# Kernel optimization log

Measured on AMD Instinct MI355X. Metric: run time of the kernel, lower is better.

The kernel has to match this reference:

```python
import jax, jax.numpy as jnp
import numpy as np

N = 50000
E = 500000
R = 8
IN_DIM = 128
HID = 128
NUM_CLASSES = 16
NUM_GRAPHS = 64


def setup_inputs() -> dict:
    key = jax.random.key(0)
    ks = jax.random.split(key, 12)
    x = jax.random.normal(ks[0], (N, IN_DIM), dtype=jnp.float32)
    edge_index = jax.random.randint(ks[1], (2, E), 0, N)
    edge_type = jax.random.randint(ks[2], (E,), 0, R)
    batch = jnp.sort(jax.random.randint(ks[3], (N,), 0, NUM_GRAPHS))
    s = 1.0 / np.sqrt(IN_DIM)
    W1 = jax.random.uniform(ks[4], (R, IN_DIM, HID), minval=-s, maxval=s, dtype=jnp.float32)
    root1 = jax.random.uniform(ks[5], (IN_DIM, HID), minval=-s, maxval=s, dtype=jnp.float32)
    b1 = jnp.zeros((HID,), jnp.float32)
    s2 = 1.0 / np.sqrt(HID)
    W2 = jax.random.uniform(ks[6], (R, HID, HID), minval=-s2, maxval=s2, dtype=jnp.float32)
    root2 = jax.random.uniform(ks[7], (HID, HID), minval=-s2, maxval=s2, dtype=jnp.float32)
    b2 = jnp.zeros((HID,), jnp.float32)
    linW = jax.random.uniform(ks[8], (HID, NUM_CLASSES), minval=-s2, maxval=s2, dtype=jnp.float32)
    linb = jnp.zeros((NUM_CLASSES,), jnp.float32)
    return {"x": x, "edge_index": edge_index, "edge_type": edge_type, "batch": batch,
            "W1": W1, "root1": root1, "b1": b1, "W2": W2, "root2": root2, "b2": b2,
            "linW": linW, "linb": linb}


def rgcn_conv(x, src, dst, rel, W, root, b):
    # Per-relation transform of ALL nodes once: [R, N, H] (avoids per-edge weight gather)
    xW = jnp.einsum('nd,rdh->rnh', x, W)
    msg = xW[rel, src]                      # [E, H] gather per edge
    # PyG RGCNConv default aggr='mean': mean over neighbors per (dst, relation)
    seg = dst * R + rel                     # composite segment id
    cnt = jax.ops.segment_sum(jnp.ones((msg.shape[0],), msg.dtype), seg, num_segments=N * R)
    norm = 1.0 / jnp.maximum(cnt, 1.0)
    msg = msg * norm[seg][:, None]
    agg = jax.ops.segment_sum(msg, dst, num_segments=N)  # sum over relations folds in
    return agg + x @ root + b


def global_mean_pool(x, batch):
    sums = jax.ops.segment_sum(x, batch, num_segments=NUM_GRAPHS)
    cnt = jax.ops.segment_sum(jnp.ones((x.shape[0],), x.dtype), batch, num_segments=NUM_GRAPHS)
    return sums / jnp.maximum(cnt, 1.0)[:, None]


def reference(x, edge_index, edge_type, batch, W1, root1, b1, W2, root2, b2, linW, linb):
    src, dst = edge_index[0], edge_index[1]
    h = jax.nn.relu(rgcn_conv(x, src, dst, edge_type, W1, root1, b1))
    h = jax.nn.relu(rgcn_conv(h, src, dst, edge_type, W2, root2, b2))
    pooled = global_mean_pool(h, batch)     # [G, HID]
    return pooled @ linW + linb             # [G, NUM_CLASSES]
```

## Files before the change

### kernel.cpp

```cpp
#include <hip/hip_runtime.h>
#include <hip/hip_bf16.h>
#include <stdint.h>

#define N_NODES 50000
#define N_EDGES 500000
#define R_REL 8
#define HID 128
#define KIN 128
#define KOUT 1152
#define N8 400000
#define NUM_GRAPHS 64
#define NUM_CLASSES 16

#define BN 32
#define LDA 1160
#define NBLK 1563

typedef __attribute__((ext_vector_type(8))) short bf16x8;
typedef __attribute__((ext_vector_type(4))) float f32x4;

__device__ __forceinline__ uint16_t f2bf(float f) {
  uint32_t u = __float_as_uint(f);
  u += 0x7FFFu + ((u >> 16) & 1u);
  return (uint16_t)(u >> 16);
}
__device__ __forceinline__ float bf2f(uint32_t b) {
  return __uint_as_float(b << 16);
}
__device__ __forceinline__ uint32_t pack2bf(float a, float b) {
  return (uint32_t)f2bf(a) | ((uint32_t)f2bf(b) << 16);
}
#define MFMA(a, b, c) __builtin_amdgcn_mfma_f32_16x16x32_bf16((a), (b), (c), 0, 0, 0)

#define HIST_B 1954
#define BND_B 196
#define WP_B 72
#define CVT_B 3125
__global__ __launch_bounds__(256) void k_prep(const int* __restrict__ ei, const int* __restrict__ et,
                                              int* __restrict__ deg8,
                                              const int* __restrict__ batch,
                                              int* __restrict__ gs, int* __restrict__ ge,
                                              const float* __restrict__ W1, const float* __restrict__ root1,
                                              uint16_t* __restrict__ Wf1,
                                              const float* __restrict__ W2, const float* __restrict__ root2,
                                              uint16_t* __restrict__ Wf2,
                                              const float* __restrict__ x, uint16_t* __restrict__ xb) {
  int b = blockIdx.x;
  int t = threadIdx.x;
  if (b < HIST_B) {
    int i = b * 256 + t;
    if (i < N_EDGES) atomicAdd(&deg8[ei[N_EDGES + i] * R_REL + et[i]], 1);
    return;
  }
  b -= HIST_B;
  if (b < BND_B) {
    int i = b * 256 + t;
    if (i < N_NODES) {
      int g = batch[i];
      if (i == 0) gs[g] = 0;
      else { int pg = batch[i - 1]; if (pg != g) { ge[pg] = i; gs[g] = i; } }
      if (i == N_NODES - 1) ge[g] = N_NODES;
    }
    return;
  }
  b -= BND_B;
  if (b < WP_B) {
    __shared__ float lw[32 * 129];
    const float* W    = (b < 36) ? W1 : W2;
    const float* root = (b < 36) ? root1 : root2;
    uint16_t*    Wf   = (b < 36) ? Wf1 : Wf2;
    int kc = (b < 36) ? b : b - 36;
    #pragma unroll
    for (int j = 0; j < 4; ++j) {
      int fi = j * 256 + t;
      int row = fi >> 5, c4 = fi & 31;
      int kk = kc * 32 + row;
      int s = kk >> 7, k = kk & 127;
      const float* src = (s < R_REL) ? (W + ((size_t)s * KIN + k) * HID) : (root + (size_t)k * HID);
      float4 v = *(const float4*)(src + c4 * 4);
      lw[row * 129 + c4 * 4 + 0] = v.x;
      lw[row * 129 + c4 * 4 + 1] = v.y;
      lw[row * 129 + c4 * 4 + 2] = v.z;
      lw[row * 129 + c4 * 4 + 3] = v.w;
    }
    __syncthreads();
    #pragma unroll
    for (int p = 0; p < 2; ++p) {
      int slot = p * 256 + t;
      int nt = slot >> 6, L = slot & 63;
      int quad = L >> 4, l16 = L & 15;
      uint16_t tmp[8];
      #pragma unroll
      for (int e = 0; e < 8; ++e)
        tmp[e] = f2bf(lw[(quad * 8 + e) * 129 + nt * 16 + l16]);
      uint4 o;
      o.x = (uint32_t)tmp[0] | ((uint32_t)tmp[1] << 16);
      o.y = (uint32_t)tmp[2] | ((uint32_t)tmp[3] << 16);
      o.z = (uint32_t)tmp[4] | ((uint32_t)tmp[5] << 16);
      o.w = (uint32_t)tmp[6] | ((uint32_t)tmp[7] << 16);
      *(uint4*)(Wf + ((size_t)(kc * 8 + nt) * 512 + (size_t)L * 8)) = o;
    }
    return;
  }
  b -= WP_B;
  {
    int i = b * 256 + t;
    const float4* p = (const float4*)x + (size_t)i * 2;
    float4 a = p[0], c = p[1];
    uint4 o;
    o.x = pack2bf(a.x, a.y); o.y = pack2bf(a.z, a.w);
    o.z = pack2bf(c.x, c.y); o.w = pack2bf(c.z, c.w);
    *(uint4*)(xb + (size_t)i * 8) = o;
  }
}

__global__ __launch_bounds__(256) void k_scan1(const int* __restrict__ deg8, int* __restrict__ offs8,
                                               int* __restrict__ bsum) {
  __shared__ int sh[256];
  int t = threadIdx.x;
  int base = blockIdx.x * 1024 + t * 4;
  int v[4]; int s = 0;
  #pragma unroll
  for (int i = 0; i < 4; ++i) { int idx = base + i; v[i] = (idx < N8) ? deg8[idx] : 0; s += v[i]; }
  sh[t] = s;
  __syncthreads();
  for (int d = 1; d < 256; d <<= 1) {
    int add = (t >= d) ? sh[t - d] : 0;
    __syncthreads();
    sh[t] += add;
    __syncthreads();
  }
  int run = sh[t] - s;
  if (t == 255) bsum[blockIdx.x] = sh[255];
  #pragma unroll
  for (int i = 0; i < 4; ++i) { int idx = base + i; if (idx < N8) offs8[idx] = run; run += v[i]; }
}

__global__ __launch_bounds__(512) void k_scan2(int* __restrict__ bsum, int nb) {
  __shared__ int sh[512];
  int t = threadIdx.x;
  int v = (t < nb) ? bsum[t] : 0;
  sh[t] = v;
  __syncthreads();
  for (int d = 1; d < 512; d <<= 1) {
    int add = (t >= d) ? sh[t - d] : 0;
    __syncthreads();
    sh[t] += add;
    __syncthreads();
  }
  if (t < nb) bsum[t] = sh[t] - v;
}

__global__ __launch_bounds__(256) void k_scan3(int* __restrict__ offs8, int* __restrict__ nxt,
                                               const int* __restrict__ bsum) {
  int i = blockIdx.x * 256 + threadIdx.x;
  if (i < N8) {
    int o = offs8[i] + bsum[i >> 10];
    offs8[i] = o;
    nxt[i] = o;
  }
  if (i == 0) offs8[N8] = N_EDGES;
}

__global__ __launch_bounds__(256) void k_scatter(const int* __restrict__ ei, const int* __restrict__ et,
                                                 int* __restrict__ nxt, uint32_t* __restrict__ epack) {
  int i = blockIdx.x * 256 + threadIdx.x;
  if (i < N_EDGES) {
    int rel = et[i];
    int dst = ei[N_EDGES + i];
    int p = atomicAdd(&nxt[dst * R_REL + rel], 1);
    epack[p] = (uint32_t)ei[i] | ((uint32_t)rel << 16) | ((uint32_t)(dst & 31) << 19);
  }
}

template<int MODE>
__global__ __launch_bounds__(512, 4) void k_fused(const uint16_t* __restrict__ hin,
                                                  const uint32_t* __restrict__ epack,
                                                  const int* __restrict__ offs8,
                                                  const uint16_t* __restrict__ Wf,
                                                  const float* __restrict__ bias,
                                                  void* __restrict__ hout,
                                                  float* __restrict__ psum,
                                                  const int* __restrict__ batch) {
  __shared__ __align__(16) uint16_t As[BN * LDA];
  int t = threadIdx.x;
  int w = __builtin_amdgcn_readfirstlane(t >> 6);
  int L = t & 63;
  int quad = L >> 4, l16 = L & 15;
  int node0 = blockIdx.x * BN;
  int voff = 2 * L;

  {
    bf16x8 z = 0;
    #pragma unroll
    for (int i = 0; i < 9; ++i) ((bf16x8*)As)[i * 512 + t] = z;
    if (t < 32) ((bf16x8*)As)[9 * 512 + t] = z;
  }

  const uint16_t* wp = Wf + (size_t)w * 512 + (size_t)L * 8;
  bf16x8 b0 = *(const bf16x8*)(wp);
  bf16x8 b1 = *(const bf16x8*)(wp + 1 * 4096);
  bf16x8 b2 = *(const bf16x8*)(wp + 2 * 4096);
  bf16x8 b3 = *(const bf16x8*)(wp + 3 * 4096);

  __syncthreads();

  #pragma unroll
  for (int ni = 0; ni < 4; ++ni) {
    int r = w * 4 + ni;
    int n = node0 + r;
    if (n < N_NODES)
      *(uint32_t*)(As + (size_t)r * LDA + R_REL * HID + voff) =
          *(const uint32_t*)(hin + (size_t)n * HID + voff);
  }

  {
    int s0 = offs8[(size_t)node0 * R_REL];
    int s1 = offs8[(size_t)min(node0 + BN, N_NODES) * R_REL];
    int ce = s1 - s0;
    int e0 = s0 + ((ce * w) >> 3);
    int e1 = s0 + ((ce * (w + 1)) >> 3);
    uint32_t kskip = 0xFFFFFFFEu;
    if (e0 > s0) kskip = epack[e0 - 1] >> 16;
    uint32_t cur = 0xFFFFFFFFu;
    float ax = 0.f, ay = 0.f; int ct = 0;
    bool done = false;
    int lsel = L & 15;
    uint32_t pv = epack[e0 + lsel];
    #pragma unroll 1
    for (int g = e0; g < s1 && !done; g += 16) {
      uint32_t pc = pv;
      int m = min(16, s1 - g);
      pv = epack[g + 16 + lsel];
      uint32_t sv[16], vv[16];
      #pragma unroll
      for (int i = 0; i < 16; ++i)
        sv[i] = (uint32_t)__builtin_amdgcn_readlane((int)pc, i);
      #pragma unroll
      for (int i = 0; i < 16; ++i) {
        uint32_t src = sv[i] & 0xFFFFu;
        src = (src < (uint32_t)N_NODES) ? src : 0u;
        vv[i] = *(const uint32_t*)(hin + (size_t)src * HID + voff);
      }
      #pragma unroll
      for (int i = 0; i < 16; ++i) {
        if (i >= m) break;
        uint32_t k = sv[i] >> 16;
        if (k == cur) {
          uint32_t v = vv[i];
          ax += bf2f(v & 0xFFFFu); ay += bf2f(v >> 16); ++ct;
        } else if (k != kskip) {
          if (cur != 0xFFFFFFFFu) {
            float iv = __builtin_amdgcn_rcpf((float)ct);
            *(uint32_t*)(As + (size_t)(cur >> 3) * LDA + (cur & 7u) * HID + voff) =
                pack2bf(ax * iv, ay * iv);
          }
          if (g + i >= e1) { done = true; cur = 0xFFFFFFFFu; break; }
          cur = k;
          uint32_t v = vv[i];
          ax = bf2f(v & 0xFFFFu); ay = bf2f(v >> 16); ct = 1;
        }
      }
    }
    if (cur != 0xFFFFFFFFu) {
      float iv = __builtin_amdgcn_rcpf((float)ct);
      *(uint32_t*)(As + (size_t)(cur >> 3) * LDA + (cur & 7u) * HID + voff) =
          pack2bf(ax * iv, ay * iv);
    }
  }
  __syncthreads();

  f32x4 acc0 = (f32x4){0.f, 0.f, 0.f, 0.f};
  f32x4 acc1 = (f32x4){0.f, 0.f, 0.f, 0.f};
  const uint16_t* ap = As + l16 * LDA + quad * 8;

  bf16x8 a0 = *(const bf16x8*)(ap);
  bf16x8 a1 = *(const bf16x8*)(ap + 16 * LDA);

  #pragma unroll 1
  for (int kc = 0; kc < 32; kc += 4) {
    bf16x8 n0, n1, nb;
    n0 = *(const bf16x8*)(ap + (kc + 1) * 32);
    n1 = *(const bf16x8*)(ap + (kc + 1) * 32 + 16 * LDA);
    nb = *(const bf16x8*)(wp + (size_t)(kc + 4) * 4096);
    acc0 = MFMA(a0, b0, acc0);
    acc1 = MFMA(a1, b0, acc1);
    a0 = n0; a1 = n1; b0 = nb;
    n0 = *(const bf16x8*)(ap + (kc + 2) * 32);
    n1 = *(const bf16x8*)(ap + (kc + 2) * 32 + 16 * LDA);
    nb = *(const bf16x8*)(wp + (size_t)(kc + 5) * 4096);
    acc0 = MFMA(a0, b1, acc0);
    acc1 = MFMA(a1, b1, acc1);
    a0 = n0; a1 = n1; b1 = nb;
    n0 = *(const bf16x8*)(ap + (kc + 3) * 32);
    n1 = *(const bf16x8*)(ap + (kc + 3) * 32 + 16 * LDA);
    nb = *(const bf16x8*)(wp + (size_t)(kc + 6) * 4096);
    acc0 = MFMA(a0, b2, acc0);
    acc1 = MFMA(a1, b2, acc1);
    a0 = n0; a1 = n1; b2 = nb;
    n0 = *(const bf16x8*)(ap + (kc + 4) * 32);
    n1 = *(const bf16x8*)(ap + (kc + 4) * 32 + 16 * LDA);
    nb = *(const bf16x8*)(wp + (size_t)(kc + 7) * 4096);
    acc0 = MFMA(a0, b3, acc0);
    acc1 = MFMA(a1, b3, acc1);
    a0 = n0; a1 = n1; b3 = nb;
  }
  {
    bf16x8 n0, n1;
    n0 = *(const bf16x8*)(ap + 33 * 32);
    n1 = *(const bf16x8*)(ap + 33 * 32 + 16 * LDA);
    acc0 = MFMA(a0, b0, acc0);
    acc1 = MFMA(a1, b0, acc1);
    a0 = n0; a1 = n1;
    n0 = *(const bf16x8*)(ap + 34 * 32);
    n1 = *(const bf16x8*)(ap + 34 * 32 + 16 * LDA);
    acc0 = MFMA(a0, b1, acc0);
    acc1 = MFMA(a1, b1, acc1);
    a0 = n0; a1 = n1;
    n0 = *(const bf16x8*)(ap + 35 * 32);
    n1 = *(const bf16x8*)(ap + 35 * 32 + 16 * LDA);
    acc0 = MFMA(a0, b2, acc0);
    acc1 = MFMA(a1, b2, acc1);
    a0 = n0; a1 = n1;
    acc0 = MFMA(a0, b3, acc0);
    acc1 = MFMA(a1, b3, acc1);
  }

  int col = w * 16 + l16;
  float bv = bias[col];
  if (MODE == 0) {
    #pragma unroll
    for (int rg = 0; rg < 4; ++rg) {
      int row = node0 + quad * 4 + rg;
      if (row < N_NODES)
        ((uint16_t*)hout)[(size_t)row * HID + col] = f2bf(fmaxf(acc0[rg] + bv, 0.f));
    }
    #pragma unroll
    for (int rg = 0; rg < 4; ++rg) {
      int row = node0 + 16 + quad * 4 + rg;
      if (row < N_NODES)
        ((uint16_t*)hout)[(size_t)row * HID + col] = f2bf(fmaxf(acc1[rg] + bv, 0.f));
    }
  } else {
    bool fast = false;
    int gA = 0;
    if (node0 + BN <= N_NODES) {
      gA = batch[node0];
      int gB = batch[node0 + BN - 1];
      fast = (gA == gB);
    }
    if (fast) {
      float s = 0.f;
      #pragma unroll
      for (int rg = 0; rg < 4; ++rg) s += fmaxf(acc0[rg] + bv, 0.f);
      #pragma unroll
      for (int rg = 0; rg < 4; ++rg) s += fmaxf(acc1[rg] + bv, 0.f);
      s += __shfl_xor(s, 16);
      s += __shfl_xor(s, 32);
      if (quad == 0) atomicAdd(&psum[gA * HID + col], s);
    } else {
      int gp = -1; float run = 0.f;
      #pragma unroll
      for (int k = 0; k < 8; ++k) {
        int rg = k & 3;
        int row = node0 + (k >> 2) * 16 + quad * 4 + rg;
        float v = (k < 4) ? acc0[rg] : acc1[rg];
        if (row < N_NODES) {
          int gg = batch[row];
          if (gg != gp) {
            if (gp >= 0) atomicAdd(&psum[gp * HID + col], run);
            run = 0.f; gp = gg;
          }
          run += fmaxf(v + bv, 0.f);
        }
      }
      if (gp >= 0) atomicAdd(&psum[gp * HID + col], run);
    }
  }
}

__global__ __launch_bounds__(1024) void k_final(const float* __restrict__ psum,
                                                const int* __restrict__ gs, const int* __restrict__ ge,
                                                const float* __restrict__ linW, const float* __restrict__ linb,
                                                float* __restrict__ out) {
  __shared__ float lp[NUM_GRAPHS * HID];
  __shared__ float lw[HID * NUM_CLASSES];
  int i = threadIdx.x;
  #pragma unroll
  for (int j = 0; j < 8; ++j) lp[j * 1024 + i] = psum[j * 1024 + i];
  #pragma unroll
  for (int j = 0; j < 2; ++j) lw[j * 1024 + i] = linW[j * 1024 + i];
  __syncthreads();
  int g = i >> 4, c = i & 15;
  float inv = 1.f / fmaxf((float)(ge[g] - gs[g]), 1.f);
  float s = 0.f;
  #pragma unroll 8
  for (int k = 0; k < HID; ++k) s += lp[g * HID + k] * lw[k * NUM_CLASSES + c];
  out[i] = s * inv + linb[c];
}

extern "C" void kernel_launch(void* const* d_in, const int* in_sizes, int n_in,
                              void* d_out, int out_size, void* d_ws, size_t ws_size,
                              hipStream_t stream) {
  const float* x     = (const float*)d_in[0];
  const int*   ei    = (const int*)d_in[1];
  const int*   et    = (const int*)d_in[2];
  const int*   batch = (const int*)d_in[3];
  const float* W1    = (const float*)d_in[4];
  const float* root1 = (const float*)d_in[5];
  const float* b1    = (const float*)d_in[6];
  const float* W2    = (const float*)d_in[7];
  const float* root2 = (const float*)d_in[8];
  const float* b2    = (const float*)d_in[9];
  const float* linW  = (const float*)d_in[10];
  const float* linb  = (const float*)d_in[11];
  float* out = (float*)d_out;

  char* ws = (char*)d_ws;
  size_t off = 0;
  auto alloc = [&](size_t bytes) -> char* {
    char* p = ws + off;
    off += (bytes + 255) & ~(size_t)255;
    return p;
  };
  int*      deg8  = (int*)alloc((size_t)N8 * 4);
  int*      gb    = (int*)alloc(2 * NUM_GRAPHS * 4);
  float*    psum  = (float*)alloc((size_t)NUM_GRAPHS * HID * 4);
  size_t zbytes = (size_t)N8 * 4 + 512 + (size_t)NUM_GRAPHS * HID * 4;
  int*      gs    = gb;
  int*      ge    = gb + NUM_GRAPHS;
  int*      offs8 = (int*)alloc((size_t)(N8 + 1) * 4);
  int*      nxt   = (int*)alloc((size_t)N8 * 4);
  int*      bsum  = (int*)alloc(512 * 4);
  uint32_t* epack = (uint32_t*)alloc((size_t)(N_EDGES + 64) * 4);
  uint16_t* Wf1   = (uint16_t*)alloc((size_t)KOUT * KIN * 2);
  uint16_t* Wf2   = (uint16_t*)alloc((size_t)KOUT * KIN * 2);
  uint16_t* xb    = (uint16_t*)alloc((size_t)N_NODES * HID * 2);
  uint16_t* h1b   = (uint16_t*)alloc((size_t)N_NODES * HID * 2);

  hipMemsetAsync(deg8, 0, zbytes, stream);

  int nb = (N8 + 1023) / 1024;
  k_prep<<<HIST_B + BND_B + WP_B + CVT_B, 256, 0, stream>>>(
      ei, et, deg8, batch, gs, ge, W1, root1, Wf1, W2, root2, Wf2, x, xb);
  k_scan1<<<nb, 256, 0, stream>>>(deg8, offs8, bsum);
  k_scan2<<<1, 512, 0, stream>>>(bsum, nb);
  k_scan3<<<(N8 + 255) / 256, 256, 0, stream>>>(offs8, nxt, bsum);
  k_scatter<<<(N_EDGES + 255) / 256, 256, 0, stream>>>(ei, et, nxt, epack);

  k_fused<0><<<NBLK, 512, 0, stream>>>(xb,  epack, offs8, Wf1, b1, h1b, nullptr, nullptr);
  k_fused<1><<<NBLK, 512, 0, stream>>>(h1b, epack, offs8, Wf2, b2, nullptr, psum, batch);

  k_final<<<1, 1024, 0, stream>>>(psum, gs, ge, linW, linb, out);
}
```

Measured before the change: 282.1 us.

## Double fused-kernel block to 16 waves with split-K GEMM and merge scan kernels

The fused gather+GEMM kernel now launches 1024 threads per block. Edge gathering is split across 16 waves instead of 8, and the 36-step K loop is split in half between two wave groups. The halves are reduced through shared memory before the epilogue. The scan2/scan3 kernels are merged into one, where each block recomputes its prefix from bsum with a wave reduction, removing one launch. This trades an extra shared-memory reduction and barrier, plus redundant prefix work per block, for more parallelism in the latency-bound gather phase.

```diff
diff --git a/kernel.cpp b/kernel.cpp
--- a/kernel.cpp
+++ b/kernel.cpp
@@ -136,26 +136,21 @@
   for (int i = 0; i < 4; ++i) { int idx = base + i; if (idx < N8) offs8[idx] = run; run += v[i]; }
 }
 
-__global__ __launch_bounds__(512) void k_scan2(int* __restrict__ bsum, int nb) {
-  __shared__ int sh[512];
+__global__ __launch_bounds__(256) void k_scan23(int* __restrict__ offs8, int* __restrict__ nxt,
+                                                const int* __restrict__ bsum, int nb) {
+  __shared__ int red[4];
   int t = threadIdx.x;
-  int v = (t < nb) ? bsum[t] : 0;
-  sh[t] = v;
-  __syncthreads();
-  for (int d = 1; d < 512; d <<= 1) {
-    int add = (t >= d) ? sh[t - d] : 0;
-    __syncthreads();
-    sh[t] += add;
-    __syncthreads();
-  }
-  if (t < nb) bsum[t] = sh[t] - v;
-}
-
-__global__ __launch_bounds__(256) void k_scan3(int* __restrict__ offs8, int* __restrict__ nxt,
-                                               const int* __restrict__ bsum) {
-  int i = blockIdx.x * 256 + threadIdx.x;
+  int blk = blockIdx.x >> 2;
+  int pre = 0;
+  for (int j = t; j < blk; j += 256) pre += bsum[j];
+  #pragma unroll
+  for (int d = 1; d < 64; d <<= 1) pre += __shfl_xor(pre, d);
+  if ((t & 63) == 0) red[t >> 6] = pre;
+  __syncthreads();
+  int total = red[0] + red[1] + red[2] + red[3];
+  int i = blockIdx.x * 256 + t;
   if (i < N8) {
-    int o = offs8[i] + bsum[i >> 10];
+    int o = offs8[i] + total;
     offs8[i] = o;
     nxt[i] = o;
   }
@@ -174,14 +169,14 @@
 }
 
 template<int MODE>
-__global__ __launch_bounds__(512, 4) void k_fused(const uint16_t* __restrict__ hin,
-                                                  const uint32_t* __restrict__ epack,
-                                                  const int* __restrict__ offs8,
-                                                  const uint16_t* __restrict__ Wf,
-                                                  const float* __restrict__ bias,
-                                                  void* __restrict__ hout,
-                                                  float* __restrict__ psum,
-                                                  const int* __restrict__ batch) {
+__global__ __launch_bounds__(1024, 4) void k_fused(const uint16_t* __restrict__ hin,
+                                                   const uint32_t* __restrict__ epack,
+                                                   const int* __restrict__ offs8,
+                                                   const uint16_t* __restrict__ Wf,
+                                                   const float* __restrict__ bias,
+                                                   void* __restrict__ hout,
+                                                   float* __restrict__ psum,
+                                                   const int* __restrict__ batch) {
   __shared__ __align__(16) uint16_t As[BN * LDA];
   int t = threadIdx.x;
   int w = __builtin_amdgcn_readfirstlane(t >> 6);
@@ -189,25 +184,24 @@
   int quad = L >> 4, l16 = L & 15;
   int node0 = blockIdx.x * BN;
   int voff = 2 * L;
+  int nt = w & 7, kh = w >> 3;
 
   {
     bf16x8 z = 0;
     #pragma unroll
-    for (int i = 0; i < 9; ++i) ((bf16x8*)As)[i * 512 + t] = z;
-    if (t < 32) ((bf16x8*)As)[9 * 512 + t] = z;
-  }
-
-  const uint16_t* wp = Wf + (size_t)w * 512 + (size_t)L * 8;
-  bf16x8 b0 = *(const bf16x8*)(wp);
-  bf16x8 b1 = *(const bf16x8*)(wp + 1 * 4096);
-  bf16x8 b2 = *(const bf16x8*)(wp + 2 * 4096);
-  bf16x8 b3 = *(const bf16x8*)(wp + 3 * 4096);
-
-  __syncthreads();
-
-  #pragma unroll
-  for (int ni = 0; ni < 4; ++ni) {
-    int r = w * 4 + ni;
+    for (int i = 0; i < 4; ++i) ((bf16x8*)As)[i * 1024 + t] = z;
+    if (t < 544) ((bf16x8*)As)[4 * 1024 + t] = z;
+  }
+
+  const uint16_t* wpk = Wf + ((size_t)(kh * 18 * 8 + nt)) * 512 + (size_t)L * 8;
+  bf16x8 b0 = *(const bf16x8*)(wpk);
+  bf16x8 b1 = *(const bf16x8*)(wpk + 4096);
+
+  __syncthreads();
+
+  #pragma unroll
+  for (int ni = 0; ni < 2; ++ni) {
+    int r = w * 2 + ni;
     int n = node0 + r;
     if (n < N_NODES)
       *(uint32_t*)(As + (size_t)r * LDA + R_REL * HID + voff) =
@@ -218,8 +212,8 @@
     int s0 = offs8[(size_t)node0 * R_REL];
     int s1 = offs8[(size_t)min(node0 + BN, N_NODES) * R_REL];
     int ce = s1 - s0;
-    int e0 = s0 + ((ce * w) >> 3);
-    int e1 = s0 + ((ce * (w + 1)) >> 3);
+    int e0 = s0 + ((ce * w) >> 4);
+    int e1 = s0 + ((ce * (w + 1)) >> 4);
     uint32_t kskip = 0xFFFFFFFEu;
     if (e0 > s0) kskip = epack[e0 - 1] >> 16;
     uint32_t cur = 0xFFFFFFFFu;
@@ -272,109 +266,96 @@
 
   f32x4 acc0 = (f32x4){0.f, 0.f, 0.f, 0.f};
   f32x4 acc1 = (f32x4){0.f, 0.f, 0.f, 0.f};
-  const uint16_t* ap = As + l16 * LDA + quad * 8;
-
-  bf16x8 a0 = *(const bf16x8*)(ap);
-  bf16x8 a1 = *(const bf16x8*)(ap + 16 * LDA);
-
-  #pragma unroll 1
-  for (int kc = 0; kc < 32; kc += 4) {
-    bf16x8 n0, n1, nb;
-    n0 = *(const bf16x8*)(ap + (kc + 1) * 32);
-    n1 = *(const bf16x8*)(ap + (kc + 1) * 32 + 16 * LDA);
-    nb = *(const bf16x8*)(wp + (size_t)(kc + 4) * 4096);
-    acc0 = MFMA(a0, b0, acc0);
-    acc1 = MFMA(a1, b0, acc1);
-    a0 = n0; a1 = n1; b0 = nb;
-    n0 = *(const bf16x8*)(ap + (kc + 2) * 32);
-    n1 = *(const bf16x8*)(ap + (kc + 2) * 32 + 16 * LDA);
-    nb = *(const bf16x8*)(wp + (size_t)(kc + 5) * 4096);
-    acc0 = MFMA(a0, b1, acc0);
-    acc1 = MFMA(a1, b1, acc1);
-    a0 = n0; a1 = n1; b1 = nb;
-    n0 = *(const bf16x8*)(ap + (kc + 3) * 32);
-    n1 = *(const bf16x8*)(ap + (kc + 3) * 32 + 16 * LDA);
-    nb = *(const bf16x8*)(wp + (size_t)(kc + 6) * 4096);
-    acc0 = MFMA(a0, b2, acc0);
-    acc1 = MFMA(a1, b2, acc1);
-    a0 = n0; a1 = n1; b2 = nb;
-    n0 = *(const bf16x8*)(ap + (kc + 4) * 32);
-    n1 = *(const bf16x8*)(ap + (kc + 4) * 32 + 16 * LDA);
-    nb = *(const bf16x8*)(wp + (size_t)(kc + 7) * 4096);
-    acc0 = MFMA(a0, b3, acc0);
-    acc1 = MFMA(a1, b3, acc1);
-    a0 = n0; a1 = n1; b3 = nb;
-  }
   {
-    bf16x8 n0, n1;
-    n0 = *(const bf16x8*)(ap + 33 * 32);
-    n1 = *(const bf16x8*)(ap + 33 * 32 + 16 * LDA);
-    acc0 = MFMA(a0, b0, acc0);
-    acc1 = MFMA(a1, b0, acc1);
-    a0 = n0; a1 = n1;
-    n0 = *(const bf16x8*)(ap + 34 * 32);
-    n1 = *(const bf16x8*)(ap + 34 * 32 + 16 * LDA);
-    acc0 = MFMA(a0, b1, acc0);
-    acc1 = MFMA(a1, b1, acc1);
-    a0 = n0; a1 = n1;
-    n0 = *(const bf16x8*)(ap + 35 * 32);
-    n1 = *(const bf16x8*)(ap + 35 * 32 + 16 * LDA);
-    acc0 = MFMA(a0, b2, acc0);
-    acc1 = MFMA(a1, b2, acc1);
-    a0 = n0; a1 = n1;
-    acc0 = MFMA(a0, b3, acc0);
-    acc1 = MFMA(a1, b3, acc1);
-  }
-
-  int col = w * 16 + l16;
-  float bv = bias[col];
-  if (MODE == 0) {
-    #pragma unroll
-    for (int rg = 0; rg < 4; ++rg) {
-      int row = node0 + quad * 4 + rg;
-      if (row < N_NODES)
-        ((uint16_t*)hout)[(size_t)row * HID + col] = f2bf(fmaxf(acc0[rg] + bv, 0.f));
-    }
-    #pragma unroll
-    for (int rg = 0; rg < 4; ++rg) {
-      int row = node0 + 16 + quad * 4 + rg;
-      if (row < N_NODES)
-        ((uint16_t*)hout)[(size_t)row * HID + col] = f2bf(fmaxf(acc1[rg] + bv, 0.f));
-    }
-  } else {
-    bool fast = false;
-    int gA = 0;
-    if (node0 + BN <= N_NODES) {
-      gA = batch[node0];
-      int gB = batch[node0 + BN - 1];
-      fast = (gA == gB);
-    }
-    if (fast) {
-      float s = 0.f;
-      #pragma unroll
-      for (int rg = 0; rg < 4; ++rg) s += fmaxf(acc0[rg] + bv, 0.f);
-      #pragma unroll
-      for (int rg = 0; rg < 4; ++rg) s += fmaxf(acc1[rg] + bv, 0.f);
-      s += __shfl_xor(s, 16);
-      s += __shfl_xor(s, 32);
-      if (quad == 0) atomicAdd(&psum[gA * HID + col], s);
+    const uint16_t* apk = As + (size_t)l16 * LDA + quad * 8 + kh * 18 * 32;
+    bf16x8 a00 = *(const bf16x8*)(apk);
+    bf16x8 a01 = *(const bf16x8*)(apk + 16 * LDA);
+    #pragma unroll 1
+    for (int kc = 0; kc < 16; kc += 2) {
+      bf16x8 nb0 = *(const bf16x8*)(wpk + (size_t)(kc + 2) * 4096);
+      bf16x8 na0 = *(const bf16x8*)(apk + (kc + 1) * 32);
+      bf16x8 na1 = *(const bf16x8*)(apk + (kc + 1) * 32 + 16 * LDA);
+      acc0 = MFMA(a00, b0, acc0);
+      acc1 = MFMA(a01, b0, acc1);
+      b0 = nb0;
+      bf16x8 nb1 = *(const bf16x8*)(wpk + (size_t)(kc + 3) * 4096);
+      bf16x8 ma0 = *(const bf16x8*)(apk + (kc + 2) * 32);
+      bf16x8 ma1 = *(const bf16x8*)(apk + (kc + 2) * 32 + 16 * LDA);
+      acc0 = MFMA(na0, b1, acc0);
+      acc1 = MFMA(na1, b1, acc1);
+      b1 = nb1; a00 = ma0; a01 = ma1;
+    }
+    bf16x8 ta0 = *(const bf16x8*)(apk + 17 * 32);
+    bf16x8 ta1 = *(const bf16x8*)(apk + 17 * 32 + 16 * LDA);
+    acc0 = MFMA(a00, b0, acc0);
+    acc1 = MFMA(a01, b0, acc1);
+    acc0 = MFMA(ta0, b1, acc0);
+    acc1 = MFMA(ta1, b1, acc1);
+  }
+
+  float* scratch = (float*)As;
+  __syncthreads();
+  if (kh == 1) {
+    float* sp = scratch + (size_t)(nt * 2) * 256 + L * 4;
+    *(f32x4*)(sp) = acc0;
+    *(f32x4*)(sp + 256) = acc1;
+  }
+  __syncthreads();
+  if (kh == 0) {
+    const float* sp = scratch + (size_t)(nt * 2) * 256 + L * 4;
+    acc0 += *(const f32x4*)(sp);
+    acc1 += *(const f32x4*)(sp + 256);
+
+    int col = nt * 16 + l16;
+    float bv = bias[col];
+    if (MODE == 0) {
+      #pragma unroll
+      for (int rg = 0; rg < 4; ++rg) {
+        int row = node0 + quad * 4 + rg;
+        if (row < N_NODES)
+          ((uint16_t*)hout)[(size_t)row * HID + col] = f2bf(fmaxf(acc0[rg] + bv, 0.f));
+      }
+      #pragma unroll
+      for (int rg = 0; rg < 4; ++rg) {
+        int row = node0 + 16 + quad * 4 + rg;
+        if (row < N_NODES)
+          ((uint16_t*)hout)[(size_t)row * HID + col] = f2bf(fmaxf(acc1[rg] + bv, 0.f));
+      }
     } else {
-      int gp = -1; float run = 0.f;
-      #pragma unroll
-      for (int k = 0; k < 8; ++k) {
-        int rg = k & 3;
-        int row = node0 + (k >> 2) * 16 + quad * 4 + rg;
-        float v = (k < 4) ? acc0[rg] : acc1[rg];
-        if (row < N_NODES) {
-          int gg = batch[row];
-          if (gg != gp) {
-            if (gp >= 0) atomicAdd(&psum[gp * HID + col], run);
-            run = 0.f; gp = gg;
+      bool fast = false;
+      int gA = 0;
+      if (node0 + BN <= N_NODES) {
+        gA = batch[node0];
+        int gB = batch[node0 + BN - 1];
+        fast = (gA == gB);
+      }
+      if (fast) {
+        float s = 0.f;
+        #pragma unroll
+        for (int rg = 0; rg < 4; ++rg) s += fmaxf(acc0[rg] + bv, 0.f);
+        #pragma unroll
+        for (int rg = 0; rg < 4; ++rg) s += fmaxf(acc1[rg] + bv, 0.f);
+        s += __shfl_xor(s, 16);
+        s += __shfl_xor(s, 32);
+        if (quad == 0) atomicAdd(&psum[gA * HID + col], s);
+      } else {
+        int gp = -1; float run = 0.f;
+        #pragma unroll
+        for (int k = 0; k < 8; ++k) {
+          int rg = k & 3;
+          int row = node0 + (k >> 2) * 16 + quad * 4 + rg;
+          float v = (k < 4) ? acc0[rg] : acc1[rg];
+          if (row < N_NODES) {
+            int gg = batch[row];
+            if (gg != gp) {
+              if (gp >= 0) atomicAdd(&psum[gp * HID + col], run);
+              run = 0.f; gp = gg;
+            }
+            run += fmaxf(v + bv, 0.f);
           }
-          run += fmaxf(v + bv, 0.f);
         }
-      }
-      if (gp >= 0) atomicAdd(&psum[gp * HID + col], run);
+        if (gp >= 0) atomicAdd(&psum[gp * HID + col], run);
+      }
     }
   }
 }
@@ -444,12 +425,11 @@
   k_prep<<<HIST_B + BND_B + WP_B + CVT_B, 256, 0, stream>>>(
       ei, et, deg8, batch, gs, ge, W1, root1, Wf1, W2, root2, Wf2, x, xb);
   k_scan1<<<nb, 256, 0, stream>>>(deg8, offs8, bsum);
-  k_scan2<<<1, 512, 0, stream>>>(bsum, nb);
-  k_scan3<<<(N8 + 255) / 256, 256, 0, stream>>>(offs8, nxt, bsum);
+  k_scan23<<<(N8 + 255) / 256, 256, 0, stream>>>(offs8, nxt, bsum, nb);
   k_scatter<<<(N_EDGES + 255) / 256, 256, 0, stream>>>(ei, et, nxt, epack);
 
-  k_fused<0><<<NBLK, 512, 0, stream>>>(xb,  epack, offs8, Wf1, b1, h1b, nullptr, nullptr);
-  k_fused<1><<<NBLK, 512, 0, stream>>>(h1b, epack, offs8, Wf2, b2, nullptr, psum, batch);
+  k_fused<0><<<NBLK, 1024, 0, stream>>>(xb,  epack, offs8, Wf1, b1, h1b, nullptr, nullptr);
+  k_fused<1><<<NBLK, 1024, 0, stream>>>(h1b, epack, offs8, Wf2, b2, nullptr, psum, batch);
 
   k_final<<<1, 1024, 0, stream>>>(psum, gs, ge, linW, linb, out);
 }
```

New measurement: 267.7 us. 5.1% less time.
